# Optimization experiments

Hardware: AMD Instinct MI355X
Metric: run time of the kernel (lower is better)

## Reference

```python
import jax, jax.numpy as jnp
import numpy as np

TOP_K = 4

def _silu_and_mul(gu):
    g, u = jnp.split(gu, 2, axis=-1)
    return jax.nn.silu(g) * u

def setup_inputs() -> dict:
    key = jax.random.key(0)
    ks = jax.random.split(key, 7)
    H, E, I, Is = 2048, 16, 1408, 5632
    s = 0.02
    return {
        "hidden_states": jax.random.normal(ks[0], (4, 1024, H), dtype=jnp.float32),
        "gate_w": jax.random.normal(ks[1], (E, H), dtype=jnp.float32) * s,
        "sgate_w": jax.random.normal(ks[2], (1, H), dtype=jnp.float32) * s,
        "w13": jax.random.normal(ks[3], (E, 2 * I, H), dtype=jnp.float32) * s,
        "w2": jax.random.normal(ks[4], (E, H, I), dtype=jnp.float32) * s,
        "shared_gate_up_w": jax.random.normal(ks[5], (2 * Is, H), dtype=jnp.float32) * s,
        "shared_down_w": jax.random.normal(ks[6], (H, Is), dtype=jnp.float32) * s,
    }

def reference(hidden_states, gate_w, sgate_w, w13, w2, shared_gate_up_w, shared_down_w):
    B, S, H = hidden_states.shape
    x = hidden_states.reshape(-1, H)  # [M, H]
    E = gate_w.shape[0]

    # shared expert: SiluAndMul MLP gated by sigmoid(shared_expert_gate(x))
    shared = _silu_and_mul(x @ shared_gate_up_w.T) @ shared_down_w.T
    shared = shared * jax.nn.sigmoid(x @ sgate_w.T)  # [M, H]

    # router: softmax in fp32, top-k (NOT renormalized, per original code)
    router_logits = x @ gate_w.T
    routing_weights = jax.nn.softmax(router_logits.astype(jnp.float32), axis=-1)
    topk_w, topk_ids = jax.lax.top_k(routing_weights, TOP_K)  # [M, K]

    # loop over fixed expert set via scan; every token goes through each
    # expert, masked by its routing coefficient (0 if not routed)
    def body(acc, ew):
        w13_e, w2_e, e = ew
        coef = jnp.sum(jnp.where(topk_ids == e, topk_w, 0.0), axis=-1)  # [M]
        h = _silu_and_mul(x @ w13_e.T)  # [M, I]
        acc = acc + (h @ w2_e.T).astype(jnp.float32) * coef[:, None]
        return acc, None

    init = jnp.zeros((x.shape[0], H), dtype=jnp.float32)
    sparse_out, _ = jax.lax.scan(body, init, (w13, w2, jnp.arange(E)))
    out = shared + sparse_out.astype(x.dtype)
    return out.reshape(B, S, H)
```

## Files before the change

kernel.cpp:

```cpp
#include <hip/hip_runtime.h>
#include <hip/hip_bf16.h>

#define E_NUM 16
#define TOPK 4
#define H_DIM 2048
#define I_DIM 1408
#define IS_DIM 5632
#define M_TOK 4096

typedef __attribute__((ext_vector_type(8))) short short8;
typedef __attribute__((ext_vector_type(4))) float f32x4;

static __device__ __forceinline__ unsigned short f2bf(float f) {
    unsigned int u = __float_as_uint(f);
    unsigned int r = (u + 0x7FFFu + ((u >> 16) & 1u)) >> 16;
    return (unsigned short)r;
}

static __device__ __forceinline__ void gl16(const unsigned short* g, unsigned short* l) {
    __builtin_amdgcn_global_load_lds(
        (const __attribute__((address_space(1))) unsigned int*)g,
        (__attribute__((address_space(3))) unsigned int*)l, 16, 0, 0);
}

__global__ __launch_bounds__(256) void k_router(
    const float* __restrict__ x, const float* __restrict__ gw,
    const float* __restrict__ sgw, int* __restrict__ counts,
    int* __restrict__ ltok, float* __restrict__ lcoef, float* __restrict__ sg)
{
    const int wid = threadIdx.x >> 6, lane = threadIdx.x & 63;
    const int t = blockIdx.x * 4 + wid;
    const float* xr = x + (size_t)t * H_DIM;
    float xv[32];
#pragma unroll
    for (int i = 0; i < 32; ++i) xv[i] = xr[i * 64 + lane];

    float lg[E_NUM];
    for (int e = 0; e < E_NUM; ++e) {
        const float* g = gw + (size_t)e * H_DIM;
        float s = 0.f;
#pragma unroll
        for (int i = 0; i < 32; ++i) s += xv[i] * g[i * 64 + lane];
#pragma unroll
        for (int off = 32; off; off >>= 1) s += __shfl_xor(s, off);
        lg[e] = s;
    }
    {
        float s = 0.f;
#pragma unroll
        for (int i = 0; i < 32; ++i) s += xv[i] * sgw[i * 64 + lane];
#pragma unroll
        for (int off = 32; off; off >>= 1) s += __shfl_xor(s, off);
        if (lane == 0) sg[t] = 1.f / (1.f + __expf(-s));
    }
    float mx = lg[0];
#pragma unroll
    for (int e = 1; e < E_NUM; ++e) mx = fmaxf(mx, lg[e]);
    float sum = 0.f, w[E_NUM];
#pragma unroll
    for (int e = 0; e < E_NUM; ++e) { w[e] = __expf(lg[e] - mx); sum += w[e]; }
    float inv = 1.f / sum;
#pragma unroll
    for (int e = 0; e < E_NUM; ++e) w[e] *= inv;

    if (lane == 0) {
        for (int j = 0; j < TOPK; ++j) {
            float best = -1.f; int bi = 0;
            for (int e = 0; e < E_NUM; ++e) if (w[e] > best) { best = w[e]; bi = e; }
            int pos = atomicAdd(&counts[bi], 1);
            ltok[bi * M_TOK + pos]  = t;
            lcoef[bi * M_TOK + pos] = best;
            w[bi] = -2.f;
        }
    }
}

__global__ void k_prefix(const int* __restrict__ counts, int* __restrict__ base) {
    if (threadIdx.x == 0) {
        int a = 0;
        for (int e = 0; e < E_NUM; ++e) { base[e] = a; a += counts[e]; }
        base[E_NUM] = a;
    }
}

__global__ __launch_bounds__(256) void k_cvtw(const float* __restrict__ src,
                                              unsigned short* __restrict__ dst, size_t n8)
{
    size_t stride = (size_t)gridDim.x * 256;
    for (size_t t = (size_t)blockIdx.x * 256 + threadIdx.x; t < n8; t += stride) {
        size_t i = t * 8;
        float4 a = *(const float4*)(src + i);
        float4 b = *(const float4*)(src + i + 4);
        union { unsigned short u[8]; short8 v; } o;
        o.u[0] = f2bf(a.x); o.u[1] = f2bf(a.y); o.u[2] = f2bf(a.z); o.u[3] = f2bf(a.w);
        o.u[4] = f2bf(b.x); o.u[5] = f2bf(b.y); o.u[6] = f2bf(b.z); o.u[7] = f2bf(b.w);
        *(short8*)(dst + i) = o.v;
    }
}

template<int TWOI, int NOFF>
__global__ __launch_bounds__(256) void k_cvtp(const float* __restrict__ src,
                                              unsigned short* __restrict__ dst, size_t n8)
{
    size_t stride = (size_t)gridDim.x * 256;
    for (size_t t = (size_t)blockIdx.x * 256 + threadIdx.x; t < n8; t += stride) {
        size_t i = t * 8;
        unsigned drow = (unsigned)(i >> 11);
        unsigned col  = (unsigned)(i & 2047u);
        unsigned grp = drow / (unsigned)TWOI;
        unsigned rr  = drow - grp * (unsigned)TWOI;
        unsigned q = rr >> 4, rm = rr & 15u;
        unsigned srow = ((q >> 1) << 4) + rm + ((q & 1u) ? (unsigned)NOFF : 0u);
        const float* s = src + (((size_t)grp * TWOI + srow) << 11) + col;
        float4 a = *(const float4*)s;
        float4 b = *(const float4*)(s + 4);
        union { unsigned short u[8]; short8 v; } o;
        o.u[0] = f2bf(a.x); o.u[1] = f2bf(a.y); o.u[2] = f2bf(a.z); o.u[3] = f2bf(a.w);
        o.u[4] = f2bf(b.x); o.u[5] = f2bf(b.y); o.u[6] = f2bf(b.z); o.u[7] = f2bf(b.w);
        *(short8*)(dst + i) = o.v;
    }
}

template<int MODE, int KDIM, long long BSTR, int KSPLIT>
__global__ __launch_bounds__(512, 2) void k_gemm(
    const unsigned short* __restrict__ Abase,
    const unsigned short* __restrict__ Bbase,
    void* __restrict__ outp,
    const int* __restrict__ ltok, const float* __restrict__ lcoef,
    const int* __restrict__ counts, const int* __restrict__ basearr,
    const float* __restrict__ sg)
{
    constexpr bool UP = (MODE == 0 || MODE == 2);
    constexpr int OSTR = (MODE == 0) ? IS_DIM : I_DIM;
    constexpr int KCH = KDIM / KSPLIT;
    constexpr int NT = KCH / 64;

    extern __shared__ unsigned short smem[];
    unsigned short* sA = smem;
    unsigned short* sB = smem + 32768;

    const int tid = threadIdx.x;
    const int lane = tid & 63, wid = tid >> 6;
    const int wr = wid >> 2, wcol = wid & 3;
    const int lr = lane & 15, lk = lane >> 4;

    const unsigned gx = gridDim.x, gy = gridDim.y;
    const unsigned nwg = gx * gy;
    const unsigned orig = blockIdx.y * gx + blockIdx.x;
    const unsigned q8 = nwg >> 3, r8 = nwg & 7;
    const unsigned xcd = orig & 7, off8 = orig >> 3;
    const unsigned wg = ((xcd < r8) ? xcd * (q8 + 1) : r8 * (q8 + 1) + (xcd - r8) * q8) + off8;
    const int n0 = (int)(wg / gy) * 256;
    const int r0 = (int)(wg % gy) * 256;
    const int e  = blockIdx.z;

    int cnt = M_TOK, gbase = 0;
    if constexpr (MODE == 2 || MODE == 3) {
        cnt = counts[e];
        if (r0 >= cnt) return;
        gbase = basearr[e];
    }
    const int kbeg = (KSPLIT > 1) ? e * KCH : 0;
    const unsigned short* Bexp = Bbase + (size_t)e * (size_t)BSTR;

    const unsigned short* aptr[2][2];
    const unsigned short* bptr[2][2];
#pragma unroll
    for (int h = 0; h < 2; ++h) {
#pragma unroll
        for (int i = 0; i < 2; ++i) {
            const int eo = (i * 512 + tid) * 8;
            const int prow = eo >> 6;
            const int kch = ((eo >> 3) & 7) ^ (prow & 7);
            const int lrow = h * 128 + prow;
            int ar;
            if constexpr (MODE == 0 || MODE == 1) ar = r0 + lrow;
            else {
                int rr2 = r0 + lrow; if (rr2 > cnt - 1) rr2 = cnt - 1;
                ar = (MODE == 2) ? ltok[e * M_TOK + rr2] : (gbase + rr2);
            }
            aptr[h][i] = Abase + (size_t)ar * KDIM + kbeg + kch * 8;
            bptr[h][i] = Bexp + (size_t)(n0 + lrow) * KDIM + kbeg + kch * 8;
        }
    }

    f32x4 acc[8][4];
    const f32x4 z = {0.f, 0.f, 0.f, 0.f};
#pragma unroll
    for (int m = 0; m < 8; ++m)
#pragma unroll
        for (int n = 0; n < 4; ++n) acc[m][n] = z;

    auto STAGEA = [&](int h, int buf, int kt) {
#pragma unroll
        for (int i = 0; i < 2; ++i)
            gl16(aptr[h][i] + kt, &sA[buf * 16384 + h * 8192 + (i * 512 + tid) * 8]);
    };
    auto STAGEB = [&](int h, int buf, int kt) {
#pragma unroll
        for (int i = 0; i < 2; ++i)
            gl16(bptr[h][i] + kt, &sB[buf * 16384 + h * 8192 + (i * 512 + tid) * 8]);
    };

    STAGEA(0, 0, 0); STAGEB(0, 0, 0); STAGEB(1, 0, 0); STAGEA(1, 0, 0);
    asm volatile("s_waitcnt vmcnt(4)" ::: "memory");
    __builtin_amdgcn_s_barrier();

    short8 af[8], bfA[4], bfB[4];

#pragma unroll 1
    for (int t = 0; t < NT; ++t) {
        const int cur = t & 1, nxt = cur ^ 1;
        const int kt1 = (t + 1) * 64;
        const bool pf = (t + 1 < NT);
        const int cb = cur * 16384;

#pragma unroll
        for (int m = 0; m < 4; ++m) {
            const int row = wr * 64 + m * 16 + lr;
#pragma unroll
            for (int kk = 0; kk < 2; ++kk)
                af[m * 2 + kk] = *(const short8*)&sA[cb + (row << 6) + ((((kk << 2) + lk) ^ (row & 7)) << 3)];
        }
#pragma unroll
        for (int n = 0; n < 2; ++n) {
            const int row = wcol * 32 + n * 16 + lr;
#pragma unroll
            for (int kk = 0; kk < 2; ++kk)
                bfA[n * 2 + kk] = *(const short8*)&sB[cb + (row << 6) + ((((kk << 2) + lk) ^ (row & 7)) << 3)];
        }
        if (pf) { STAGEA(0, nxt, kt1); STAGEB(0, nxt, kt1); }
        __builtin_amdgcn_s_setprio(1);
#pragma unroll
        for (int kk = 0; kk < 2; ++kk)
#pragma unroll
            for (int n = 0; n < 2; ++n)
#pragma unroll
                for (int m = 0; m < 4; ++m)
                    acc[m][n] = __builtin_amdgcn_mfma_f32_16x16x32_bf16(af[m * 2 + kk], bfA[n * 2 + kk], acc[m][n], 0, 0, 0);
        __builtin_amdgcn_s_setprio(0);
        if (pf) asm volatile("s_waitcnt vmcnt(4)" ::: "memory");
        else    asm volatile("s_waitcnt vmcnt(0)" ::: "memory");
        __builtin_amdgcn_s_barrier();

#pragma unroll
        for (int n = 0; n < 2; ++n) {
            const int row = 128 + wcol * 32 + n * 16 + lr;
#pragma unroll
            for (int kk = 0; kk < 2; ++kk)
                bfB[n * 2 + kk] = *(const short8*)&sB[cb + (row << 6) + ((((kk << 2) + lk) ^ (row & 7)) << 3)];
        }
        if (pf) { STAGEB(1, nxt, kt1); STAGEA(1, nxt, kt1); }
        __builtin_amdgcn_s_setprio(1);
#pragma unroll
        for (int kk = 0; kk < 2; ++kk)
#pragma unroll
            for (int n = 0; n < 2; ++n)
#pragma unroll
                for (int m = 0; m < 4; ++m)
                    acc[m][n + 2] = __builtin_amdgcn_mfma_f32_16x16x32_bf16(af[m * 2 + kk], bfB[n * 2 + kk], acc[m][n + 2], 0, 0, 0);
        __builtin_amdgcn_s_setprio(0);

#pragma unroll
        for (int m = 0; m < 4; ++m) {
            const int row = 128 + wr * 64 + m * 16 + lr;
#pragma unroll
            for (int kk = 0; kk < 2; ++kk)
                af[m * 2 + kk] = *(const short8*)&sA[cb + (row << 6) + ((((kk << 2) + lk) ^ (row & 7)) << 3)];
        }
        __builtin_amdgcn_s_setprio(1);
#pragma unroll
        for (int kk = 0; kk < 2; ++kk)
#pragma unroll
            for (int n = 0; n < 2; ++n)
#pragma unroll
                for (int m = 0; m < 4; ++m)
                    acc[m + 4][n] = __builtin_amdgcn_mfma_f32_16x16x32_bf16(af[m * 2 + kk], bfA[n * 2 + kk], acc[m + 4][n], 0, 0, 0);
#pragma unroll
        for (int kk = 0; kk < 2; ++kk)
#pragma unroll
            for (int n = 0; n < 2; ++n)
#pragma unroll
                for (int m = 0; m < 4; ++m)
                    acc[m + 4][n + 2] = __builtin_amdgcn_mfma_f32_16x16x32_bf16(af[m * 2 + kk], bfB[n * 2 + kk], acc[m + 4][n + 2], 0, 0, 0);
        __builtin_amdgcn_s_setprio(0);
        asm volatile("s_waitcnt vmcnt(4)" ::: "memory");
        __builtin_amdgcn_s_barrier();
    }

    if constexpr (UP) {
        const int hc0 = (n0 >> 1) + wcol * 16 + lr;
        unsigned short* hb = (unsigned short*)outp;
#pragma unroll
        for (int m = 0; m < 8; ++m) {
            const int rb = (m < 4 ? wr * 64 + m * 16 : 128 + wr * 64 + (m - 4) * 16) + lk * 4;
#pragma unroll
            for (int j = 0; j < 4; ++j) {
                const int r = rb + j;
                bool ok; size_t orow;
                if constexpr (MODE == 0) { ok = true; orow = (size_t)(r0 + r) * OSTR; }
                else { ok = (r0 + r < cnt); orow = (size_t)(gbase + r0 + r) * OSTR; }
                if (ok) {
                    float g0 = acc[m][0][j], u0 = acc[m][1][j];
                    float g1 = acc[m][2][j], u1 = acc[m][3][j];
                    hb[orow + hc0]      = f2bf(g0 / (1.f + __expf(-g0)) * u0);
                    hb[orow + hc0 + 64] = f2bf(g1 / (1.f + __expf(-g1)) * u1);
                }
            }
        }
    } else {
        float* op = (float*)outp;
#pragma unroll
        for (int m = 0; m < 8; ++m) {
            const int rb = (m < 4 ? wr * 64 + m * 16 : 128 + wr * 64 + (m - 4) * 16) + lk * 4;
#pragma unroll
            for (int j = 0; j < 4; ++j) {
                const int r = rb + j;
                int tok; float scale; bool ok;
                if constexpr (MODE == 1) {
                    tok = r0 + r; scale = sg[tok]; ok = true;
                } else {
                    ok = (r0 + r < cnt);
                    int idx = ok ? (e * M_TOK + r0 + r) : (e * M_TOK);
                    tok = ltok[idx]; scale = lcoef[idx];
                }
                if (ok) {
                    size_t orow = (size_t)tok * H_DIM;
#pragma unroll
                    for (int n = 0; n < 4; ++n) {
                        const int col = n0 + (n < 2 ? wcol * 32 + n * 16 : 128 + wcol * 32 + (n - 2) * 16) + lr;
                        atomicAdd(op + orow + col, acc[m][n][j] * scale);
                    }
                }
            }
        }
    }
}

extern "C" void kernel_launch(void* const* d_in, const int* in_sizes, int n_in,
                              void* d_out, int out_size, void* d_ws, size_t ws_size,
                              hipStream_t stream) {
    const float* x    = (const float*)d_in[0];
    const float* gw   = (const float*)d_in[1];
    const float* sgw  = (const float*)d_in[2];
    const float* w13  = (const float*)d_in[3];
    const float* w2   = (const float*)d_in[4];
    const float* sguw = (const float*)d_in[5];
    const float* sdw  = (const float*)d_in[6];
    float* out = (float*)d_out;

    char* ws = (char*)d_ws;
    unsigned short* xb    = (unsigned short*)ws;
    unsigned short* hbuf  = (unsigned short*)(ws + 16777216);
    unsigned short* w13b  = (unsigned short*)(ws + 62914560);
    unsigned short* w2b   = (unsigned short*)(ws + 247463936);
    unsigned short* sguwb = (unsigned short*)(ws + 339738624);
    unsigned short* sdwb  = (unsigned short*)(ws + 385875968);
    size_t so = 408944640ULL;
    int*   ltok   = (int*)  (ws + so);
    float* lcoef  = (float*)(ws + so + 262144);
    int*   counts = (int*)  (ws + so + 524288);
    int*   basep  = (int*)  (ws + so + 524288 + 256);
    float* sg     = (float*)(ws + so + 524288 + 512);

    hipMemsetAsync(counts, 0, 64, stream);
    hipMemsetAsync(out, 0, (size_t)out_size * sizeof(float), stream);
    k_router<<<M_TOK / 4, 256, 0, stream>>>(x, gw, sgw, counts, ltok, lcoef, sg);
    k_prefix<<<1, 64, 0, stream>>>(counts, basep);
    k_cvtw<<<4096, 256, 0, stream>>>(x, xb, (size_t)M_TOK * H_DIM / 8);
    k_cvtp<2 * IS_DIM, IS_DIM><<<8192, 256, 0, stream>>>(sguw, sguwb, (size_t)2 * IS_DIM * H_DIM / 8);
    k_cvtw<<<8192, 256, 0, stream>>>(sdw,  sdwb,  (size_t)H_DIM * IS_DIM / 8);
    k_cvtp<2 * I_DIM, I_DIM><<<8192, 256, 0, stream>>>(w13, w13b, (size_t)E_NUM * 2 * I_DIM * H_DIM / 8);
    k_cvtw<<<8192, 256, 0, stream>>>(w2,   w2b,   (size_t)E_NUM * H_DIM * I_DIM / 8);

    static const int DYN = 131072;
    (void)hipFuncSetAttribute(reinterpret_cast<const void*>(&k_gemm<0, 2048, 0LL, 1>),
                              hipFuncAttributeMaxDynamicSharedMemorySize, DYN);
    (void)hipFuncSetAttribute(reinterpret_cast<const void*>(&k_gemm<1, 5632, 0LL, 2>),
                              hipFuncAttributeMaxDynamicSharedMemorySize, DYN);
    (void)hipFuncSetAttribute(reinterpret_cast<const void*>(&k_gemm<2, 2048, 5767168LL, 1>),
                              hipFuncAttributeMaxDynamicSharedMemorySize, DYN);
    (void)hipFuncSetAttribute(reinterpret_cast<const void*>(&k_gemm<3, 1408, 2883584LL, 1>),
                              hipFuncAttributeMaxDynamicSharedMemorySize, DYN);

    k_gemm<0, 2048, 0LL, 1>
        <<<dim3(2 * IS_DIM / 256, M_TOK / 256, 1), 512, DYN, stream>>>(
            xb, sguwb, hbuf, ltok, lcoef, counts, basep, sg);
    k_gemm<1, 5632, 0LL, 2>
        <<<dim3(H_DIM / 256, M_TOK / 256, 2), 512, DYN, stream>>>(
            hbuf, sdwb, out, ltok, lcoef, counts, basep, sg);
    k_gemm<2, 2048, 5767168LL, 1>
        <<<dim3(2 * I_DIM / 256, M_TOK / 256, E_NUM), 512, DYN, stream>>>(
            xb, w13b, hbuf, ltok, lcoef, counts, basep, sg);
    k_gemm<3, 1408, 2883584LL, 1>
        <<<dim3(H_DIM / 256, M_TOK / 256, E_NUM), 512, DYN, stream>>>(
            hbuf, w2b, out, ltok, lcoef, counts, basep, sg);
}
```

Before: 1.215 ms.

## Switch GEMM to 256x128 tiles with a three-stage LDS pipeline

Halves the N dimension of each workgroup tile from 256 to 128 and doubles the grid along N. Each wave now computes a 64x64 sub-tile instead of a split 128x64. The double-buffered half-tile staging is replaced by a three-buffer ring that prefetches two k-steps ahead with one barrier per iteration. This aims to cut accumulator register pressure, barrier count and load latency. In exchange it lowers MFMA work per LDS read and raises shared memory per block to 144KB, which limits each CU to one block.

```diff
diff --git a/kernel.cpp b/kernel.cpp
--- a/kernel.cpp
+++ b/kernel.cpp
@@ -137,11 +137,11 @@
 
     extern __shared__ unsigned short smem[];
     unsigned short* sA = smem;
-    unsigned short* sB = smem + 32768;
+    unsigned short* sB = smem + 49152;
 
     const int tid = threadIdx.x;
     const int lane = tid & 63, wid = tid >> 6;
-    const int wr = wid >> 2, wcol = wid & 3;
+    const int wr = wid >> 1, wc = wid & 1;
     const int lr = lane & 15, lk = lane >> 4;
 
     const unsigned gx = gridDim.x, gy = gridDim.y;
@@ -150,7 +150,7 @@
     const unsigned q8 = nwg >> 3, r8 = nwg & 7;
     const unsigned xcd = orig & 7, off8 = orig >> 3;
     const unsigned wg = ((xcd < r8) ? xcd * (q8 + 1) : r8 * (q8 + 1) + (xcd - r8) * q8) + off8;
-    const int n0 = (int)(wg / gy) * 256;
+    const int n0 = (int)(wg / gy) * 128;
     const int r0 = (int)(wg % gy) * 256;
     const int e  = blockIdx.z;
 
@@ -164,7 +164,6 @@
     const unsigned short* Bexp = Bbase + (size_t)e * (size_t)BSTR;
 
     const unsigned short* aptr[2][2];
-    const unsigned short* bptr[2][2];
 #pragma unroll
     for (int h = 0; h < 2; ++h) {
 #pragma unroll
@@ -180,123 +179,92 @@
                 ar = (MODE == 2) ? ltok[e * M_TOK + rr2] : (gbase + rr2);
             }
             aptr[h][i] = Abase + (size_t)ar * KDIM + kbeg + kch * 8;
-            bptr[h][i] = Bexp + (size_t)(n0 + lrow) * KDIM + kbeg + kch * 8;
-        }
-    }
-
-    f32x4 acc[8][4];
+        }
+    }
+    const unsigned short* bptr[2];
+#pragma unroll
+    for (int i = 0; i < 2; ++i) {
+        const int eo = (i * 512 + tid) * 8;
+        const int prow = eo >> 6;
+        const int kch = ((eo >> 3) & 7) ^ (prow & 7);
+        bptr[i] = Bexp + (size_t)(n0 + prow) * KDIM + kbeg + kch * 8;
+    }
+
+    f32x4 acc[4][4];
     const f32x4 z = {0.f, 0.f, 0.f, 0.f};
 #pragma unroll
-    for (int m = 0; m < 8; ++m)
+    for (int m = 0; m < 4; ++m)
 #pragma unroll
         for (int n = 0; n < 4; ++n) acc[m][n] = z;
 
-    auto STAGEA = [&](int h, int buf, int kt) {
+    auto STAGE = [&](int buf, int kt) {
 #pragma unroll
         for (int i = 0; i < 2; ++i)
-            gl16(aptr[h][i] + kt, &sA[buf * 16384 + h * 8192 + (i * 512 + tid) * 8]);
+            gl16(aptr[0][i] + kt, &sA[buf * 16384 + (i * 512 + tid) * 8]);
+#pragma unroll
+        for (int i = 0; i < 2; ++i)
+            gl16(aptr[1][i] + kt, &sA[buf * 16384 + 8192 + (i * 512 + tid) * 8]);
+#pragma unroll
+        for (int i = 0; i < 2; ++i)
+            gl16(bptr[i] + kt, &sB[buf * 8192 + (i * 512 + tid) * 8]);
     };
-    auto STAGEB = [&](int h, int buf, int kt) {
-#pragma unroll
-        for (int i = 0; i < 2; ++i)
-            gl16(bptr[h][i] + kt, &sB[buf * 16384 + h * 8192 + (i * 512 + tid) * 8]);
-    };
-
-    STAGEA(0, 0, 0); STAGEB(0, 0, 0); STAGEB(1, 0, 0); STAGEA(1, 0, 0);
-    asm volatile("s_waitcnt vmcnt(4)" ::: "memory");
+
+    STAGE(0, 0);
+    STAGE(1, 64);
+    asm volatile("s_waitcnt vmcnt(6)" ::: "memory");
     __builtin_amdgcn_s_barrier();
 
-    short8 af[8], bfA[4], bfB[4];
+    short8 af[8], bf[8];
+    int rb = 0;
 
 #pragma unroll 1
     for (int t = 0; t < NT; ++t) {
-        const int cur = t & 1, nxt = cur ^ 1;
-        const int kt1 = (t + 1) * 64;
-        const bool pf = (t + 1 < NT);
-        const int cb = cur * 16384;
+        const bool pf = (t + 2 < NT);
+        int wb = rb + 2; if (wb >= 3) wb -= 3;
+        const int cbA = rb * 16384, cbB = rb * 8192;
 
 #pragma unroll
         for (int m = 0; m < 4; ++m) {
             const int row = wr * 64 + m * 16 + lr;
 #pragma unroll
             for (int kk = 0; kk < 2; ++kk)
-                af[m * 2 + kk] = *(const short8*)&sA[cb + (row << 6) + ((((kk << 2) + lk) ^ (row & 7)) << 3)];
-        }
-#pragma unroll
-        for (int n = 0; n < 2; ++n) {
-            const int row = wcol * 32 + n * 16 + lr;
+                af[m * 2 + kk] = *(const short8*)&sA[cbA + (row << 6) + ((((kk << 2) + lk) ^ (row & 7)) << 3)];
+        }
+#pragma unroll
+        for (int n = 0; n < 4; ++n) {
+            const int row = wc * 64 + n * 16 + lr;
 #pragma unroll
             for (int kk = 0; kk < 2; ++kk)
-                bfA[n * 2 + kk] = *(const short8*)&sB[cb + (row << 6) + ((((kk << 2) + lk) ^ (row & 7)) << 3)];
-        }
-        if (pf) { STAGEA(0, nxt, kt1); STAGEB(0, nxt, kt1); }
+                bf[n * 2 + kk] = *(const short8*)&sB[cbB + (row << 6) + ((((kk << 2) + lk) ^ (row & 7)) << 3)];
+        }
+
+        if (pf) STAGE(wb, (t + 2) * 64);
+
         __builtin_amdgcn_s_setprio(1);
 #pragma unroll
         for (int kk = 0; kk < 2; ++kk)
 #pragma unroll
-            for (int n = 0; n < 2; ++n)
+            for (int n = 0; n < 4; ++n)
 #pragma unroll
                 for (int m = 0; m < 4; ++m)
-                    acc[m][n] = __builtin_amdgcn_mfma_f32_16x16x32_bf16(af[m * 2 + kk], bfA[n * 2 + kk], acc[m][n], 0, 0, 0);
+                    acc[m][n] = __builtin_amdgcn_mfma_f32_16x16x32_bf16(af[m * 2 + kk], bf[n * 2 + kk], acc[m][n], 0, 0, 0);
         __builtin_amdgcn_s_setprio(0);
-        if (pf) asm volatile("s_waitcnt vmcnt(4)" ::: "memory");
+
+        if (pf) asm volatile("s_waitcnt vmcnt(6)" ::: "memory");
         else    asm volatile("s_waitcnt vmcnt(0)" ::: "memory");
         __builtin_amdgcn_s_barrier();
 
-#pragma unroll
-        for (int n = 0; n < 2; ++n) {
-            const int row = 128 + wcol * 32 + n * 16 + lr;
-#pragma unroll
-            for (int kk = 0; kk < 2; ++kk)
-                bfB[n * 2 + kk] = *(const short8*)&sB[cb + (row << 6) + ((((kk << 2) + lk) ^ (row & 7)) << 3)];
-        }
-        if (pf) { STAGEB(1, nxt, kt1); STAGEA(1, nxt, kt1); }
-        __builtin_amdgcn_s_setprio(1);
-#pragma unroll
-        for (int kk = 0; kk < 2; ++kk)
-#pragma unroll
-            for (int n = 0; n < 2; ++n)
-#pragma unroll
-                for (int m = 0; m < 4; ++m)
-                    acc[m][n + 2] = __builtin_amdgcn_mfma_f32_16x16x32_bf16(af[m * 2 + kk], bfB[n * 2 + kk], acc[m][n + 2], 0, 0, 0);
-        __builtin_amdgcn_s_setprio(0);
-
+        rb = (rb + 1 == 3) ? 0 : rb + 1;
+    }
+
+    if constexpr (UP) {
+        const int hc0 = (n0 >> 1) + wc * 32 + lr;
+        unsigned short* hb = (unsigned short*)outp;
 #pragma unroll
         for (int m = 0; m < 4; ++m) {
-            const int row = 128 + wr * 64 + m * 16 + lr;
-#pragma unroll
-            for (int kk = 0; kk < 2; ++kk)
-                af[m * 2 + kk] = *(const short8*)&sA[cb + (row << 6) + ((((kk << 2) + lk) ^ (row & 7)) << 3)];
-        }
-        __builtin_amdgcn_s_setprio(1);
-#pragma unroll
-        for (int kk = 0; kk < 2; ++kk)
-#pragma unroll
-            for (int n = 0; n < 2; ++n)
-#pragma unroll
-                for (int m = 0; m < 4; ++m)
-                    acc[m + 4][n] = __builtin_amdgcn_mfma_f32_16x16x32_bf16(af[m * 2 + kk], bfA[n * 2 + kk], acc[m + 4][n], 0, 0, 0);
-#pragma unroll
-        for (int kk = 0; kk < 2; ++kk)
-#pragma unroll
-            for (int n = 0; n < 2; ++n)
-#pragma unroll
-                for (int m = 0; m < 4; ++m)
-                    acc[m + 4][n + 2] = __builtin_amdgcn_mfma_f32_16x16x32_bf16(af[m * 2 + kk], bfB[n * 2 + kk], acc[m + 4][n + 2], 0, 0, 0);
-        __builtin_amdgcn_s_setprio(0);
-        asm volatile("s_waitcnt vmcnt(4)" ::: "memory");
-        __builtin_amdgcn_s_barrier();
-    }
-
-    if constexpr (UP) {
-        const int hc0 = (n0 >> 1) + wcol * 16 + lr;
-        unsigned short* hb = (unsigned short*)outp;
-#pragma unroll
-        for (int m = 0; m < 8; ++m) {
-            const int rb = (m < 4 ? wr * 64 + m * 16 : 128 + wr * 64 + (m - 4) * 16) + lk * 4;
 #pragma unroll
             for (int j = 0; j < 4; ++j) {
-                const int r = rb + j;
+                const int r = wr * 64 + m * 16 + lk * 4 + j;
                 bool ok; size_t orow;
                 if constexpr (MODE == 0) { ok = true; orow = (size_t)(r0 + r) * OSTR; }
                 else { ok = (r0 + r < cnt); orow = (size_t)(gbase + r0 + r) * OSTR; }
@@ -304,18 +272,17 @@
                     float g0 = acc[m][0][j], u0 = acc[m][1][j];
                     float g1 = acc[m][2][j], u1 = acc[m][3][j];
                     hb[orow + hc0]      = f2bf(g0 / (1.f + __expf(-g0)) * u0);
-                    hb[orow + hc0 + 64] = f2bf(g1 / (1.f + __expf(-g1)) * u1);
+                    hb[orow + hc0 + 16] = f2bf(g1 / (1.f + __expf(-g1)) * u1);
                 }
             }
         }
     } else {
         float* op = (float*)outp;
 #pragma unroll
-        for (int m = 0; m < 8; ++m) {
-            const int rb = (m < 4 ? wr * 64 + m * 16 : 128 + wr * 64 + (m - 4) * 16) + lk * 4;
+        for (int m = 0; m < 4; ++m) {
 #pragma unroll
             for (int j = 0; j < 4; ++j) {
-                const int r = rb + j;
+                const int r = wr * 64 + m * 16 + lk * 4 + j;
                 int tok; float scale; bool ok;
                 if constexpr (MODE == 1) {
                     tok = r0 + r; scale = sg[tok]; ok = true;
@@ -328,7 +295,7 @@
                     size_t orow = (size_t)tok * H_DIM;
 #pragma unroll
                     for (int n = 0; n < 4; ++n) {
-                        const int col = n0 + (n < 2 ? wcol * 32 + n * 16 : 128 + wcol * 32 + (n - 2) * 16) + lr;
+                        const int col = n0 + wc * 64 + n * 16 + lr;
                         atomicAdd(op + orow + col, acc[m][n][j] * scale);
                     }
                 }
@@ -373,7 +340,7 @@
     k_cvtp<2 * I_DIM, I_DIM><<<8192, 256, 0, stream>>>(w13, w13b, (size_t)E_NUM * 2 * I_DIM * H_DIM / 8);
     k_cvtw<<<8192, 256, 0, stream>>>(w2,   w2b,   (size_t)E_NUM * H_DIM * I_DIM / 8);
 
-    static const int DYN = 131072;
+    static const int DYN = 147456;
     (void)hipFuncSetAttribute(reinterpret_cast<const void*>(&k_gemm<0, 2048, 0LL, 1>),
                               hipFuncAttributeMaxDynamicSharedMemorySize, DYN);
     (void)hipFuncSetAttribute(reinterpret_cast<const void*>(&k_gemm<1, 5632, 0LL, 2>),
@@ -384,15 +351,15 @@
                               hipFuncAttributeMaxDynamicSharedMemorySize, DYN);
 
     k_gemm<0, 2048, 0LL, 1>
-        <<<dim3(2 * IS_DIM / 256, M_TOK / 256, 1), 512, DYN, stream>>>(
+        <<<dim3(2 * IS_DIM / 128, M_TOK / 256, 1), 512, DYN, stream>>>(
             xb, sguwb, hbuf, ltok, lcoef, counts, basep, sg);
     k_gemm<1, 5632, 0LL, 2>
-        <<<dim3(H_DIM / 256, M_TOK / 256, 2), 512, DYN, stream>>>(
+        <<<dim3(H_DIM / 128, M_TOK / 256, 2), 512, DYN, stream>>>(
             hbuf, sdwb, out, ltok, lcoef, counts, basep, sg);
     k_gemm<2, 2048, 5767168LL, 1>
-        <<<dim3(2 * I_DIM / 256, M_TOK / 256, E_NUM), 512, DYN, stream>>>(
+        <<<dim3(2 * I_DIM / 128, M_TOK / 256, E_NUM), 512, DYN, stream>>>(
             xb, w13b, hbuf, ltok, lcoef, counts, basep, sg);
     k_gemm<3, 1408, 2883584LL, 1>
-        <<<dim3(H_DIM / 256, M_TOK / 256, E_NUM), 512, DYN, stream>>>(
+        <<<dim3(H_DIM / 128, M_TOK / 256, E_NUM), 512, DYN, stream>>>(
             hbuf, w2b, out, ltok, lcoef, counts, basep, sg);
 }
```

After: 1.197 ms (median of 2 runs). No clear change (-1.5%).
